# Kernel tuning notes

Hardware: AMD Instinct MI355X
Metric: run time of the kernel (lower is better)

## Reference

```python
import jax, jax.numpy as jnp
import numpy as np

TEMPERATURE = 0.07
BN_EPS = 1e-5
NORM_EPS = 1e-12


def _forward_features(x, conv_w, conv_b, gamma, beta, lin_w, lin_b):
    # prepend_relu
    x = jax.nn.relu(x)
    # 1x1 conv: [B, Cin, H, W] x [Cout, Cin] -> [B, Cout, H, W]
    x = jnp.einsum('bihw,oi->bohw', x, conv_w) + conv_b[None, :, None, None]
    # BatchNorm2d, training mode (biased batch stats over N,H,W per channel)
    mu = x.mean(axis=(0, 2, 3))
    var = x.var(axis=(0, 2, 3))
    x = (x - mu[None, :, None, None]) * jax.lax.rsqrt(var + BN_EPS)[None, :, None, None]
    x = x * gamma[None, :, None, None] + beta[None, :, None, None]
    x = jax.nn.relu(x)
    # second 1x1 conv ('linear')
    x = jnp.einsum('bihw,oi->bohw', x, lin_w) + lin_b[None, :, None, None]
    # append_normalize: F.normalize(p=2, dim=1)
    norm = jnp.sqrt(jnp.sum(x * x, axis=1, keepdims=True))
    x = x / jnp.maximum(norm, NORM_EPS)
    return x


def _dense_info_nce(o, t):
    # o, t: [B, C, H, W]
    B, C, H, W = t.shape
    o = o.transpose(0, 2, 3, 1).reshape(B, H * W, C)  # [B, HW, C]
    t = t.transpose(0, 2, 3, 1).reshape(B, H * W, C)
    pos = jnp.einsum('bik,bik->bi', o, t) / TEMPERATURE          # [B, HW]
    logits = jnp.einsum('bik,bjk->bij', o, t) / TEMPERATURE      # [B, HW, HW]
    lse = jax.nn.logsumexp(logits, axis=-1)                      # [B, HW]
    return jnp.mean(lse - pos)


def setup_inputs() -> dict:
    key = jax.random.key(0)
    ks = jax.random.split(key, 4)
    B, Cin, Cout, H, W = 8, 256, 128, 60, 60
    x_orig = jax.random.normal(ks[0], (B, Cin, H, W), jnp.float32)
    x_trans = jax.random.normal(ks[1], (B, Cin, H, W), jnp.float32)
    conv_w = jax.random.normal(ks[2], (Cout, Cin), jnp.float32) * (1.0 / np.sqrt(Cin))
    conv_b = jnp.zeros((Cout,), jnp.float32)
    gamma = jnp.ones((Cout,), jnp.float32)
    beta = jnp.zeros((Cout,), jnp.float32)
    lin_w = jax.random.normal(ks[3], (Cout, Cout), jnp.float32) * (1.0 / np.sqrt(Cout))
    lin_b = jnp.zeros((Cout,), jnp.float32)
    return {"x_orig": x_orig, "x_trans": x_trans, "conv_w": conv_w, "conv_b": conv_b,
            "gamma": gamma, "beta": beta, "lin_w": lin_w, "lin_b": lin_b}


def reference(x_orig, x_trans, conv_w, conv_b, gamma, beta, lin_w, lin_b):
    o = _forward_features(x_orig, conv_w, conv_b, gamma, beta, lin_w, lin_b)
    t = _forward_features(x_trans, conv_w, conv_b, gamma, beta, lin_w, lin_b)
    return _dense_info_nce(o, t)
```

## Files before the change

### kernel.cpp

```cpp
#include <hip/hip_runtime.h>
#include <hip/hip_bf16.h>

#define HW 3600
#define NQ 28800
#define CIN 256
#define CMID 128

typedef short bf16x8 __attribute__((ext_vector_type(8)));
typedef float f32x4 __attribute__((ext_vector_type(4)));

#define INV_T 14.285714285714286f
#define SQRT_INV_T 3.7796447300922722f
#define LOG2E 1.4426950408889634f
#define NM (-20.60992915555662f)

__device__ inline unsigned short f2bf(float f) {
  unsigned u = __float_as_uint(f);
  return (unsigned short)((u + 0x7fffu + ((u >> 16) & 1u)) >> 16);
}
__device__ inline float bf2f(unsigned short h) { return __uint_as_float((unsigned)h << 16); }

__global__ void prep_kernel(const float* __restrict__ conv_w, const float* __restrict__ lin_w,
                            unsigned short* __restrict__ cw16, unsigned short* __restrict__ lw16) {
  const int i = blockIdx.x * 256 + threadIdx.x;
  if (i < 128 * 256) cw16[i] = f2bf(conv_w[i]);
  if (i < 128 * 128) lw16[i] = f2bf(lin_w[i]);
}

__global__ __launch_bounds__(256, 4) void conv1_mfma_kernel(
    const float* __restrict__ x, const unsigned short* __restrict__ cw16,
    unsigned short* __restrict__ yt, float* __restrict__ stats) {
  __shared__ __align__(16) unsigned short xT[64 * 32];
  __shared__ float sredw[4][128];
  __shared__ float s2redw[4][128];
  const int t = threadIdx.x;
  const int w = t >> 6;
  const int l = t & 63;
  const int lr = l & 15;
  const int lg = l >> 4;
  const int q0 = blockIdx.x * 64;

  f32x4 acc[8];
#pragma unroll
  for (int tile = 0; tile < 8; tile++) acc[tile] = (f32x4){0.f, 0.f, 0.f, 0.f};

  const int qcol = q0 + 4 * (t & 15);
  const int bb = qcol / HW;
  const int pp = qcol - bb * HW;
  const float* xcol = x + (size_t)bb * CIN * HW + pp;

  for (int ch = 0; ch < 8; ch++) {
    __syncthreads();
#pragma unroll
    for (int r = 0; r < 2; r++) {
      const int cil = (t >> 4) + r * 16;
      float4 v = *(const float4*)&xcol[(size_t)(ch * 32 + cil) * HW];
      unsigned short* dst = &xT[(4 * (t & 15)) * 32 + cil];
      dst[0]  = f2bf(fmaxf(v.x, 0.f));
      dst[32] = f2bf(fmaxf(v.y, 0.f));
      dst[64] = f2bf(fmaxf(v.z, 0.f));
      dst[96] = f2bf(fmaxf(v.w, 0.f));
    }
    __syncthreads();
    bf16x8 bv = *(const bf16x8*)&xT[(w * 16 + lr) * 32 + lg * 8];
#pragma unroll
    for (int tile = 0; tile < 8; tile++) {
      bf16x8 av = *(const bf16x8*)&cw16[(size_t)(tile * 16 + lr) * 256 + ch * 32 + lg * 8];
      acc[tile] = __builtin_amdgcn_mfma_f32_16x16x32_bf16(av, bv, acc[tile], 0, 0, 0);
    }
  }

#pragma unroll
  for (int tile = 0; tile < 8; tile++) {
#pragma unroll
    for (int i = 0; i < 4; i++) {
      float v = acc[tile][i];
      float v2 = v * v;
      v += __shfl_xor(v, 1); v2 += __shfl_xor(v2, 1);
      v += __shfl_xor(v, 2); v2 += __shfl_xor(v2, 2);
      v += __shfl_xor(v, 4); v2 += __shfl_xor(v2, 4);
      v += __shfl_xor(v, 8); v2 += __shfl_xor(v2, 8);
      if (lr == 0) {
        sredw[w][tile * 16 + lg * 4 + i] = v;
        s2redw[w][tile * 16 + lg * 4 + i] = v2;
      }
    }
  }

  const int q = q0 + w * 16 + lr;
#pragma unroll
  for (int tile = 0; tile < 8; tile++) {
    union { unsigned short u[4]; uint2 v; } pk;
#pragma unroll
    for (int i = 0; i < 4; i++) pk.u[i] = f2bf(acc[tile][i]);
    *(uint2*)&yt[(size_t)q * 128 + tile * 16 + lg * 4] = pk.v;
  }

  __syncthreads();
  if (t < 128) {
    atomicAdd(&stats[t], sredw[0][t] + sredw[1][t] + sredw[2][t] + sredw[3][t]);
    atomicAdd(&stats[128 + t], s2redw[0][t] + s2redw[1][t] + s2redw[2][t] + s2redw[3][t]);
  }
}

__global__ void scale_kernel(const float* __restrict__ stats, const float* __restrict__ conv_b,
                             const float* __restrict__ gamma, const float* __restrict__ beta,
                             float* __restrict__ sc) {
  const int c = threadIdx.x;
  const float inv_n = 1.f / (float)NQ;
  const float macc = stats[c] * inv_n;
  const float var = stats[128 + c] * inv_n - macc * macc;
  const float mean = macc + conv_b[c];
  const float s = gamma[c] * rsqrtf(var + 1e-5f);
  const float tt = beta[c] - mean * s;
  sc[c] = s;
  sc[128 + c] = conv_b[c] * s + tt;
}

__global__ __launch_bounds__(256, 4) void conv2_mfma_kernel(
    const unsigned short* __restrict__ yt, const unsigned short* __restrict__ lw16,
    const float* __restrict__ sc, const float* __restrict__ lin_b,
    unsigned short* __restrict__ feat) {
  const int t = threadIdx.x;
  const int w = t >> 6;
  const int l = t & 63;
  const int lr = l & 15;
  const int lg = l >> 4;
  const int q = blockIdx.x * 64 + w * 16 + lr;

  f32x4 acc[8];
#pragma unroll
  for (int tile = 0; tile < 8; tile++) acc[tile] = (f32x4){0.f, 0.f, 0.f, 0.f};

  const unsigned short* yrow = yt + (size_t)q * 128;
  for (int ch = 0; ch < 4; ch++) {
    bf16x8 raw = *(const bf16x8*)&yrow[ch * 32 + lg * 8];
    bf16x8 bv;
#pragma unroll
    for (int e = 0; e < 8; e++) {
      const int c = ch * 32 + lg * 8 + e;
      float v = fmaxf(fmaf(bf2f((unsigned short)raw[e]), sc[c], sc[128 + c]), 0.f);
      bv[e] = (short)f2bf(v);
    }
#pragma unroll
    for (int tile = 0; tile < 8; tile++) {
      bf16x8 av = *(const bf16x8*)&lw16[(size_t)(tile * 16 + lr) * 128 + ch * 32 + lg * 8];
      acc[tile] = __builtin_amdgcn_mfma_f32_16x16x32_bf16(av, bv, acc[tile], 0, 0, 0);
    }
  }

  float vals[8][4];
  float ssq = 0.f;
#pragma unroll
  for (int tile = 0; tile < 8; tile++) {
#pragma unroll
    for (int i = 0; i < 4; i++) {
      float v = acc[tile][i] + lin_b[tile * 16 + lg * 4 + i];
      vals[tile][i] = v;
      ssq += v * v;
    }
  }
  ssq += __shfl_xor(ssq, 16);
  ssq += __shfl_xor(ssq, 32);
  const float inv = SQRT_INV_T / fmaxf(sqrtf(ssq), 1e-12f);

#pragma unroll
  for (int tile = 0; tile < 8; tile++) {
    union { unsigned short u[4]; uint2 v; } pk;
#pragma unroll
    for (int i = 0; i < 4; i++) pk.u[i] = f2bf(vals[tile][i] * inv);
    *(uint2*)&feat[(size_t)q * 128 + tile * 16 + lg * 4] = pk.v;
  }
}

__global__ __launch_bounds__(256, 2) void infonce_kernel(
    const unsigned short* __restrict__ fo, const unsigned short* __restrict__ ft,
    float* __restrict__ sumexp) {
  const int b = blockIdx.z;
  const int t = threadIdx.x;
  const int w = t >> 6;
  const int lane = t & 63;
  const int lr = lane & 15;
  const int lkq = lane >> 4;
  const int base = blockIdx.x * 256 + w * 64;
  if (base >= HW) return;
  const unsigned short* fob = fo + (size_t)b * HW * 128;
  const unsigned short* ftb = ft + (size_t)b * HW * 128;

  bf16x8 a[4][4];
#pragma unroll
  for (int tile = 0; tile < 4; tile++) {
    const int r = min(base + tile * 16 + lr, HW - 1);
    const unsigned short* ap = fob + (size_t)r * 128 + lkq * 8;
#pragma unroll
    for (int kk = 0; kk < 4; kk++) a[tile][kk] = *(const bf16x8*)(ap + kk * 32);
  }
  float rs[4][4];
#pragma unroll
  for (int tile = 0; tile < 4; tile++)
#pragma unroll
    for (int i = 0; i < 4; i++) rs[tile][i] = 0.f;

  for (int ch = blockIdx.y; ch < 75; ch += 4) {
    const int cbase = ch * 48;
    bf16x8 bv[3][4];
#pragma unroll
    for (int sub = 0; sub < 3; sub++) {
      const unsigned short* bp = ftb + (size_t)(cbase + sub * 16 + lr) * 128 + lkq * 8;
#pragma unroll
      for (int kk = 0; kk < 4; kk++) bv[sub][kk] = *(const bf16x8*)(bp + kk * 32);
    }
    f32x4 acc[4][3];
#pragma unroll
    for (int tile = 0; tile < 4; tile++)
#pragma unroll
      for (int sub = 0; sub < 3; sub++) acc[tile][sub] = (f32x4){0.f, 0.f, 0.f, 0.f};
#pragma unroll
    for (int kk = 0; kk < 4; kk++)
#pragma unroll
      for (int tile = 0; tile < 4; tile++)
#pragma unroll
        for (int sub = 0; sub < 3; sub++)
          acc[tile][sub] = __builtin_amdgcn_mfma_f32_16x16x32_bf16(
              a[tile][kk], bv[sub][kk], acc[tile][sub], 0, 0, 0);
#pragma unroll
    for (int tile = 0; tile < 4; tile++)
#pragma unroll
      for (int sub = 0; sub < 3; sub++)
#pragma unroll
        for (int i = 0; i < 4; i++)
          rs[tile][i] += exp2f(fmaf(acc[tile][sub][i], LOG2E, NM));
  }
#pragma unroll
  for (int tile = 0; tile < 4; tile++)
#pragma unroll
    for (int i = 0; i < 4; i++) {
      float v = rs[tile][i];
      v += __shfl_xor(v, 1); v += __shfl_xor(v, 2);
      v += __shfl_xor(v, 4); v += __shfl_xor(v, 8);
      rs[tile][i] = v;
    }
  if (lr == 0) {
#pragma unroll
    for (int tile = 0; tile < 4; tile++)
#pragma unroll
      for (int i = 0; i < 4; i++) {
        const int r = base + tile * 16 + lkq * 4 + i;
        if (r < HW) atomicAdd(&sumexp[b * HW + r], rs[tile][i]);
      }
  }
}

__global__ __launch_bounds__(256) void final_kernel(
    const float* __restrict__ sumexp, const unsigned short* __restrict__ fo,
    const unsigned short* __restrict__ ft, float* __restrict__ out) {
  const int q = blockIdx.x * 256 + threadIdx.x;
  float val = 0.f;
  if (q < NQ) {
    const unsigned short* a = fo + (size_t)q * 128;
    const unsigned short* c = ft + (size_t)q * 128;
    float dot = 0.f;
#pragma unroll
    for (int k = 0; k < 128; k += 8) {
      bf16x8 ua = *(const bf16x8*)(a + k);
      bf16x8 ub = *(const bf16x8*)(c + k);
#pragma unroll
      for (int e = 0; e < 8; e++)
        dot = fmaf(bf2f((unsigned short)ua[e]), bf2f((unsigned short)ub[e]), dot);
    }
    val = logf(sumexp[q]) + INV_T - dot;
  }
#pragma unroll
  for (int m = 1; m < 64; m <<= 1) val += __shfl_xor(val, m);
  __shared__ float red[4];
  const int wid = threadIdx.x >> 6;
  if ((threadIdx.x & 63) == 0) red[wid] = val;
  __syncthreads();
  if (threadIdx.x == 0)
    atomicAdd(out, (red[0] + red[1] + red[2] + red[3]) * (1.f / (float)NQ));
}

extern "C" void kernel_launch(void* const* d_in, const int* in_sizes, int n_in,
                              void* d_out, int out_size, void* d_ws, size_t ws_size,
                              hipStream_t stream) {
  (void)in_sizes; (void)n_in; (void)out_size; (void)ws_size;
  const float* x_orig = (const float*)d_in[0];
  const float* x_trans = (const float*)d_in[1];
  const float* conv_w = (const float*)d_in[2];
  const float* conv_b = (const float*)d_in[3];
  const float* gamma = (const float*)d_in[4];
  const float* beta = (const float*)d_in[5];
  const float* lin_w = (const float*)d_in[6];
  const float* lin_b = (const float*)d_in[7];
  float* out = (float*)d_out;

  char* ws = (char*)d_ws;
  unsigned short* yt = (unsigned short*)(ws + 0);
  unsigned short* cw16 = (unsigned short*)(ws + 7372800);
  unsigned short* lw16 = (unsigned short*)(ws + 7438336);
  float* statsO = (float*)(ws + 7471104);
  float* statsT = (float*)(ws + 7472128);
  float* scO = (float*)(ws + 7473152);
  float* scT = (float*)(ws + 7474176);
  float* sumexp = (float*)(ws + 7475200);
  unsigned short* feat_o = (unsigned short*)(ws + 7590400);
  unsigned short* feat_t = (unsigned short*)(ws + 14963200);

  hipMemsetAsync(ws + 7471104, 0, 2048 + 2048 + 115200, stream);
  hipMemsetAsync(d_out, 0, sizeof(float), stream);

  prep_kernel<<<128, 256, 0, stream>>>(conv_w, lin_w, cw16, lw16);

  conv1_mfma_kernel<<<450, 256, 0, stream>>>(x_orig, cw16, yt, statsO);
  scale_kernel<<<1, 128, 0, stream>>>(statsO, conv_b, gamma, beta, scO);
  conv2_mfma_kernel<<<450, 256, 0, stream>>>(yt, lw16, scO, lin_b, feat_o);

  conv1_mfma_kernel<<<450, 256, 0, stream>>>(x_trans, cw16, yt, statsT);
  scale_kernel<<<1, 128, 0, stream>>>(statsT, conv_b, gamma, beta, scT);
  conv2_mfma_kernel<<<450, 256, 0, stream>>>(yt, lw16, scT, lin_b, feat_t);

  infonce_kernel<<<dim3(15, 4, 8), 256, 0, stream>>>(feat_o, feat_t, sumexp);
  final_kernel<<<113, 256, 0, stream>>>(sumexp, feat_o, feat_t, out);
}
```

Before: 278.7 us.

## Batch both branches into single launches, prefetch conv1 inputs, widen infonce grid

Runs the orig and trans feature pipelines together via a z grid dimension, so conv1, scale and conv2 each launch once with twice the blocks, and the yt scratch buffer is doubled to hold both. The conv1 input loads are software-prefetched one channel chunk ahead to overlap global loads with MFMA work. The infonce grid's y split grows from 4 to 15 so more blocks share the column chunks. This raises occupancy and cuts launch count, at the cost of more workspace and more atomic sumexp contention.

Result: faster. 258.9 us (-7.1%).

```diff
diff --git a/kernel.cpp b/kernel.cpp
--- a/kernel.cpp
+++ b/kernel.cpp
@@ -28,11 +28,17 @@
 }
 
 __global__ __launch_bounds__(256, 4) void conv1_mfma_kernel(
-    const float* __restrict__ x, const unsigned short* __restrict__ cw16,
+    const float* __restrict__ x0, const float* __restrict__ x1,
+    const unsigned short* __restrict__ cw16,
     unsigned short* __restrict__ yt, float* __restrict__ stats) {
   __shared__ __align__(16) unsigned short xT[64 * 32];
   __shared__ float sredw[4][128];
   __shared__ float s2redw[4][128];
+  const int z = blockIdx.z;
+  const float* x = z ? x1 : x0;
+  float* st = stats + z * 256;
+  unsigned short* yz = yt + (size_t)z * NQ * 128;
+
   const int t = threadIdx.x;
   const int w = t >> 6;
   const int l = t & 63;
@@ -48,20 +54,31 @@
   const int bb = qcol / HW;
   const int pp = qcol - bb * HW;
   const float* xcol = x + (size_t)bb * CIN * HW + pp;
+  const int cil0 = (t >> 4);
+  const int cil1 = cil0 + 16;
+
+  float4 v0 = *(const float4*)&xcol[(size_t)cil0 * HW];
+  float4 v1 = *(const float4*)&xcol[(size_t)cil1 * HW];
 
   for (int ch = 0; ch < 8; ch++) {
+    if (ch) __syncthreads();
+    {
+      unsigned short* dst = &xT[(4 * (t & 15)) * 32 + cil0];
+      dst[0]  = f2bf(fmaxf(v0.x, 0.f));
+      dst[32] = f2bf(fmaxf(v0.y, 0.f));
+      dst[64] = f2bf(fmaxf(v0.z, 0.f));
+      dst[96] = f2bf(fmaxf(v0.w, 0.f));
+      dst = &xT[(4 * (t & 15)) * 32 + cil1];
+      dst[0]  = f2bf(fmaxf(v1.x, 0.f));
+      dst[32] = f2bf(fmaxf(v1.y, 0.f));
+      dst[64] = f2bf(fmaxf(v1.z, 0.f));
+      dst[96] = f2bf(fmaxf(v1.w, 0.f));
+    }
     __syncthreads();
-#pragma unroll
-    for (int r = 0; r < 2; r++) {
-      const int cil = (t >> 4) + r * 16;
-      float4 v = *(const float4*)&xcol[(size_t)(ch * 32 + cil) * HW];
-      unsigned short* dst = &xT[(4 * (t & 15)) * 32 + cil];
-      dst[0]  = f2bf(fmaxf(v.x, 0.f));
-      dst[32] = f2bf(fmaxf(v.y, 0.f));
-      dst[64] = f2bf(fmaxf(v.z, 0.f));
-      dst[96] = f2bf(fmaxf(v.w, 0.f));
-    }
-    __syncthreads();
+    if (ch < 7) {
+      v0 = *(const float4*)&xcol[(size_t)((ch + 1) * 32 + cil0) * HW];
+      v1 = *(const float4*)&xcol[(size_t)((ch + 1) * 32 + cil1) * HW];
+    }
     bf16x8 bv = *(const bf16x8*)&xT[(w * 16 + lr) * 32 + lg * 8];
 #pragma unroll
     for (int tile = 0; tile < 8; tile++) {
@@ -93,34 +110,42 @@
     union { unsigned short u[4]; uint2 v; } pk;
 #pragma unroll
     for (int i = 0; i < 4; i++) pk.u[i] = f2bf(acc[tile][i]);
-    *(uint2*)&yt[(size_t)q * 128 + tile * 16 + lg * 4] = pk.v;
+    *(uint2*)&yz[(size_t)q * 128 + tile * 16 + lg * 4] = pk.v;
   }
 
   __syncthreads();
   if (t < 128) {
-    atomicAdd(&stats[t], sredw[0][t] + sredw[1][t] + sredw[2][t] + sredw[3][t]);
-    atomicAdd(&stats[128 + t], s2redw[0][t] + s2redw[1][t] + s2redw[2][t] + s2redw[3][t]);
+    atomicAdd(&st[t], sredw[0][t] + sredw[1][t] + sredw[2][t] + sredw[3][t]);
+    atomicAdd(&st[128 + t], s2redw[0][t] + s2redw[1][t] + s2redw[2][t] + s2redw[3][t]);
   }
 }
 
 __global__ void scale_kernel(const float* __restrict__ stats, const float* __restrict__ conv_b,
                              const float* __restrict__ gamma, const float* __restrict__ beta,
                              float* __restrict__ sc) {
+  const int z = blockIdx.x;
+  const float* st = stats + z * 256;
+  float* scz = sc + z * 256;
   const int c = threadIdx.x;
   const float inv_n = 1.f / (float)NQ;
-  const float macc = stats[c] * inv_n;
-  const float var = stats[128 + c] * inv_n - macc * macc;
+  const float macc = st[c] * inv_n;
+  const float var = st[128 + c] * inv_n - macc * macc;
   const float mean = macc + conv_b[c];
   const float s = gamma[c] * rsqrtf(var + 1e-5f);
   const float tt = beta[c] - mean * s;
-  sc[c] = s;
-  sc[128 + c] = conv_b[c] * s + tt;
+  scz[c] = s;
+  scz[128 + c] = conv_b[c] * s + tt;
 }
 
 __global__ __launch_bounds__(256, 4) void conv2_mfma_kernel(
     const unsigned short* __restrict__ yt, const unsigned short* __restrict__ lw16,
     const float* __restrict__ sc, const float* __restrict__ lin_b,
-    unsigned short* __restrict__ feat) {
+    unsigned short* __restrict__ feat_o, unsigned short* __restrict__ feat_t) {
+  const int z = blockIdx.z;
+  const unsigned short* yz = yt + (size_t)z * NQ * 128;
+  const float* scz = sc + z * 256;
+  unsigned short* feat = z ? feat_t : feat_o;
+
   const int t = threadIdx.x;
   const int w = t >> 6;
   const int l = t & 63;
@@ -132,14 +157,14 @@
 #pragma unroll
   for (int tile = 0; tile < 8; tile++) acc[tile] = (f32x4){0.f, 0.f, 0.f, 0.f};
 
-  const unsigned short* yrow = yt + (size_t)q * 128;
+  const unsigned short* yrow = yz + (size_t)q * 128;
   for (int ch = 0; ch < 4; ch++) {
     bf16x8 raw = *(const bf16x8*)&yrow[ch * 32 + lg * 8];
     bf16x8 bv;
 #pragma unroll
     for (int e = 0; e < 8; e++) {
       const int c = ch * 32 + lg * 8 + e;
-      float v = fmaxf(fmaf(bf2f((unsigned short)raw[e]), sc[c], sc[128 + c]), 0.f);
+      float v = fmaxf(fmaf(bf2f((unsigned short)raw[e]), scz[c], scz[128 + c]), 0.f);
       bv[e] = (short)f2bf(v);
     }
 #pragma unroll
@@ -201,7 +226,7 @@
 #pragma unroll
     for (int i = 0; i < 4; i++) rs[tile][i] = 0.f;
 
-  for (int ch = blockIdx.y; ch < 75; ch += 4) {
+  for (int ch = blockIdx.y; ch < 75; ch += 15) {
     const int cbase = ch * 48;
     bf16x8 bv[3][4];
 #pragma unroll
@@ -296,29 +321,23 @@
 
   char* ws = (char*)d_ws;
   unsigned short* yt = (unsigned short*)(ws + 0);
-  unsigned short* cw16 = (unsigned short*)(ws + 7372800);
-  unsigned short* lw16 = (unsigned short*)(ws + 7438336);
-  float* statsO = (float*)(ws + 7471104);
-  float* statsT = (float*)(ws + 7472128);
-  float* scO = (float*)(ws + 7473152);
-  float* scT = (float*)(ws + 7474176);
-  float* sumexp = (float*)(ws + 7475200);
-  unsigned short* feat_o = (unsigned short*)(ws + 7590400);
-  unsigned short* feat_t = (unsigned short*)(ws + 14963200);
-
-  hipMemsetAsync(ws + 7471104, 0, 2048 + 2048 + 115200, stream);
+  unsigned short* cw16 = (unsigned short*)(ws + 14745600);
+  unsigned short* lw16 = (unsigned short*)(ws + 14811136);
+  float* stats = (float*)(ws + 14843904);
+  float* sc = (float*)(ws + 14845952);
+  float* sumexp = (float*)(ws + 14848000);
+  unsigned short* feat_o = (unsigned short*)(ws + 14963200);
+  unsigned short* feat_t = (unsigned short*)(ws + 22336000);
+
+  hipMemsetAsync(ws + 14843904, 0, 2048 + 2048 + 115200, stream);
   hipMemsetAsync(d_out, 0, sizeof(float), stream);
 
   prep_kernel<<<128, 256, 0, stream>>>(conv_w, lin_w, cw16, lw16);
 
-  conv1_mfma_kernel<<<450, 256, 0, stream>>>(x_orig, cw16, yt, statsO);
-  scale_kernel<<<1, 128, 0, stream>>>(statsO, conv_b, gamma, beta, scO);
-  conv2_mfma_kernel<<<450, 256, 0, stream>>>(yt, lw16, scO, lin_b, feat_o);
-
-  conv1_mfma_kernel<<<450, 256, 0, stream>>>(x_trans, cw16, yt, statsT);
-  scale_kernel<<<1, 128, 0, stream>>>(statsT, conv_b, gamma, beta, scT);
-  conv2_mfma_kernel<<<450, 256, 0, stream>>>(yt, lw16, scT, lin_b, feat_t);
-
-  infonce_kernel<<<dim3(15, 4, 8), 256, 0, stream>>>(feat_o, feat_t, sumexp);
+  conv1_mfma_kernel<<<dim3(450, 1, 2), 256, 0, stream>>>(x_orig, x_trans, cw16, yt, stats);
+  scale_kernel<<<2, 128, 0, stream>>>(stats, conv_b, gamma, beta, sc);
+  conv2_mfma_kernel<<<dim3(450, 1, 2), 256, 0, stream>>>(yt, lw16, sc, lin_b, feat_o, feat_t);
+
+  infonce_kernel<<<dim3(15, 15, 8), 256, 0, stream>>>(feat_o, feat_t, sumexp);
   final_kernel<<<113, 256, 0, stream>>>(sumexp, feat_o, feat_t, out);
 }
```
